# Kernel optimization log

Hardware: AMD Instinct MI355X
Metric: run time of the kernel (lower is better)

## Reference

```python
import jax, jax.numpy as jnp
import numpy as np

N = 50000      # n_nodes
E = 800000     # n_edges
IN_CH = 128
HID = 128
OUT_CH = 64
N_LAYERS = 4


def _linear_params(key, fan_in, fan_out):
    kw, kb = jax.random.split(key)
    bound = 1.0 / np.sqrt(fan_in)
    W = jax.random.uniform(kw, (fan_out, fan_in), jnp.float32, -bound, bound)
    b = jax.random.uniform(kb, (fan_out,), jnp.float32, -bound, bound)
    return W, b


def setup_inputs() -> dict:
    key = jax.random.key(0)
    ks = jax.random.split(key, 5)
    x = jax.random.normal(ks[0], (N, IN_CH), jnp.float32)
    edge_index = jax.random.randint(ks[1], (2, E), 0, N, dtype=jnp.int64)
    W_in, b_in = _linear_params(ks[2], IN_CH, HID)
    conv_keys = jax.random.split(ks[3], N_LAYERS)
    Wc = jnp.stack([_linear_params(k, HID, HID)[0] for k in conv_keys])
    bc = jnp.stack([_linear_params(k, HID, HID)[1] for k in conv_keys])
    W_out, b_out = _linear_params(ks[4], HID * N_LAYERS, OUT_CH)
    return {"x": x, "edge_index": edge_index, "W_in": W_in, "b_in": b_in,
            "Wc": Wc, "bc": bc, "W_out": W_out, "b_out": b_out}


def reference(x, edge_index, W_in, b_in, Wc, bc, W_out, b_out):
    n = x.shape[0]
    # input projection + relu
    x = jax.nn.relu(x @ W_in.T + b_in)
    src, dst = edge_index[0], edge_index[1]
    loop = jnp.arange(n, dtype=edge_index.dtype)
    src_a = jnp.concatenate([src, loop])   # [E+N]
    dst_a = jnp.concatenate([dst, loop])   # [E+N]
    # symmetric-normalized degree (with self loops)
    deg = jax.ops.segment_sum(jnp.ones(src_a.shape[0], x.dtype), dst_a, num_segments=n)
    norm = (deg[src_a] * deg[dst_a]) ** -0.5
    norm = jnp.where(jnp.isinf(norm), 0.0, norm)  # guard deg==0 (original sets inf->0)
    layer_outputs = []
    for i in range(Wc.shape[0]):
        h = x @ Wc[i].T + bc[i]                     # [N, HID]
        msg = h[src_a] * norm[:, None]              # gather + scale  [E+N, HID]
        out = jax.ops.segment_sum(msg, dst_a, num_segments=n)  # scatter-add
        x = jax.nn.relu(out)
        layer_outputs.append(x)
    h = jnp.concatenate(layer_outputs, axis=-1)     # jk_mode='cat' -> [N, HID*L]
    return h @ W_out.T + b_out
```

## Files before the change

### kernel.cpp

```cpp
#include <hip/hip_runtime.h>
#include <hip/hip_bf16.h>

#ifndef MIN
#define MIN(a,b) ((a)<(b)?(a):(b))
#endif

typedef _Float16 half2_t __attribute__((ext_vector_type(2)));
typedef _Float16 half4_t __attribute__((ext_vector_type(4)));
typedef _Float16 half8_t __attribute__((ext_vector_type(8)));
typedef float floatx4 __attribute__((ext_vector_type(4)));

#define BUCKET_SHIFT 6
#define BUCKET_SIZE 64
#define SCHUNK 8192


__global__ void hist_kernel(const int* __restrict__ dst, int E,
                            int* __restrict__ bucketCnt, int NB) {
    __shared__ int h[1024];
    int t = threadIdx.x;
    for (int i = t; i < 1024; i += 256) h[i] = 0;
    __syncthreads();
    for (int e = blockIdx.x * 256 + t; e < E; e += gridDim.x * 256)
        atomicAdd(&h[dst[e] >> BUCKET_SHIFT], 1);
    __syncthreads();
    for (int i = t; i < NB; i += 256)
        if (h[i]) atomicAdd(&bucketCnt[i], h[i]);
}

__global__ void bucket_scan(const int* __restrict__ bucketCnt,
                            int* __restrict__ bucketBase, int* __restrict__ bucketCur,
                            int NB, int E) {
    __shared__ int sm[1024];
    int t = threadIdx.x;
    int v = (t < NB) ? bucketCnt[t] : 0;
    sm[t] = v;
    __syncthreads();
    for (int off = 1; off < 1024; off <<= 1) {
        int add = (t >= off) ? sm[t - off] : 0;
        __syncthreads();
        sm[t] += add;
        __syncthreads();
    }
    if (t < NB) {
        bucketBase[t] = sm[t] - v;
        bucketCur[t] = sm[t] - v;
    }
    if (t == 0) bucketBase[NB] = E;
}

__global__ void scatter_kernel(const int* __restrict__ src, const int* __restrict__ dst,
                               int E, int* __restrict__ bucketCur, uint2* __restrict__ rec) {
    __shared__ int hist[1024];
    __shared__ int base[1024];
    int t = threadIdx.x;
    int e0 = blockIdx.x * SCHUNK;
    int e1 = MIN(E, e0 + SCHUNK);
    for (int i = t; i < 1024; i += 256) hist[i] = 0;
    __syncthreads();
    for (int e = e0 + t; e < e1; e += 256)
        atomicAdd(&hist[dst[e] >> BUCKET_SHIFT], 1);
    __syncthreads();
    for (int i = t; i < 1024; i += 256) {
        int c = hist[i];
        base[i] = c ? atomicAdd(&bucketCur[i], c) : 0;
        hist[i] = 0;
    }
    __syncthreads();
    for (int e = e0 + t; e < e1; e += 256) {
        int d = dst[e];
        int b = d >> BUCKET_SHIFT;
        int pos = base[b] + atomicAdd(&hist[b], 1);
        rec[pos] = make_uint2((unsigned)src[e], (unsigned)d);
    }
}

__global__ void bucket_build(const uint2* __restrict__ rec, const int* __restrict__ bucketBase,
                             int* __restrict__ rowptr, int* __restrict__ csr_src,
                             float* __restrict__ dinv, int N, int E) {
    __shared__ int lcnt[256];
    __shared__ int sm[256];
    __shared__ int lcur[64];
    int b = blockIdx.x;
    int t = threadIdx.x;
    int beg = bucketBase[b], end = bucketBase[b + 1];
    lcnt[t] = 0;
    __syncthreads();
    for (int i = beg + t; i < end; i += 256)
        atomicAdd(&lcnt[rec[i].y & (BUCKET_SIZE - 1)], 1);
    __syncthreads();
    int v = lcnt[t];
    sm[t] = v;
    __syncthreads();
    for (int off = 1; off < 256; off <<= 1) {
        int add = (t >= off) ? sm[t - off] : 0;
        __syncthreads();
        sm[t] += add;
        __syncthreads();
    }
    int excl = sm[t] - v;
    if (t < BUCKET_SIZE) {
        int node = b * BUCKET_SIZE + t;
        if (node < N) {
            rowptr[node] = beg + excl;
            dinv[node] = rsqrtf((float)(v + 1));
        }
        lcur[t] = beg + excl;
    }
    __syncthreads();
    for (int i = beg + t; i < end; i += 256) {
        uint2 r = rec[i];
        int pos = atomicAdd(&lcur[r.y & (BUCKET_SIZE - 1)], 1);
        csr_src[pos] = (int)r.x;
    }
    if (b == 0 && t == 0) rowptr[N] = E;
}


__global__ void cvt_weights(const float* __restrict__ a, _Float16* __restrict__ oa, int na,
                            const float* __restrict__ b, _Float16* __restrict__ ob, int nb,
                            const float* __restrict__ c, _Float16* __restrict__ oc, int nc) {
    int i = blockIdx.x * blockDim.x + threadIdx.x;
    if (i < na) oa[i] = (_Float16)a[i];
    if (i < nb) ob[i] = (_Float16)b[i];
    if (i < nc) oc[i] = (_Float16)c[i];
}


__global__ void agg_kernel(const half2_t* __restrict__ Hb, const float* __restrict__ dinv,
                           const int* __restrict__ rowptr, const int* __restrict__ csr_src,
                           half2_t* __restrict__ X, int N) {
    int node = blockIdx.x * 4 + (threadIdx.x >> 6);
    int t = threadIdx.x & 63;
    if (node >= N) return;
    float di = dinv[node];
    half2_t hu = Hb[(size_t)node * 64 + t];
    float2 acc;
    acc.x = (float)hu.x * di;
    acc.y = (float)hu.y * di;
    int beg = rowptr[node];
    int end = rowptr[node + 1];

    for (int base = beg; base < end; base += 64) {
        int idx = base + t;
        bool valid = idx < end;
        int s_lane = valid ? csr_src[idx] : node;
        float w_lane = valid ? dinv[s_lane] : 0.0f;
        int m = end - base;
        if (m > 64) m = 64;
        int mm = (m + 7) & ~7;
        for (int j = 0; j < mm; j += 8) {
            int s0 = __shfl(s_lane, j + 0), s1 = __shfl(s_lane, j + 1);
            int s2 = __shfl(s_lane, j + 2), s3 = __shfl(s_lane, j + 3);
            int s4 = __shfl(s_lane, j + 4), s5 = __shfl(s_lane, j + 5);
            int s6 = __shfl(s_lane, j + 6), s7 = __shfl(s_lane, j + 7);
            float w0 = __shfl(w_lane, j + 0), w1 = __shfl(w_lane, j + 1);
            float w2 = __shfl(w_lane, j + 2), w3 = __shfl(w_lane, j + 3);
            float w4 = __shfl(w_lane, j + 4), w5 = __shfl(w_lane, j + 5);
            float w6 = __shfl(w_lane, j + 6), w7 = __shfl(w_lane, j + 7);
            half2_t u0 = Hb[(size_t)s0 * 64 + t];
            half2_t u1 = Hb[(size_t)s1 * 64 + t];
            half2_t u2 = Hb[(size_t)s2 * 64 + t];
            half2_t u3 = Hb[(size_t)s3 * 64 + t];
            half2_t u4 = Hb[(size_t)s4 * 64 + t];
            half2_t u5 = Hb[(size_t)s5 * 64 + t];
            half2_t u6 = Hb[(size_t)s6 * 64 + t];
            half2_t u7 = Hb[(size_t)s7 * 64 + t];
            acc.x = fmaf((float)u0.x, w0, acc.x); acc.y = fmaf((float)u0.y, w0, acc.y);
            acc.x = fmaf((float)u1.x, w1, acc.x); acc.y = fmaf((float)u1.y, w1, acc.y);
            acc.x = fmaf((float)u2.x, w2, acc.x); acc.y = fmaf((float)u2.y, w2, acc.y);
            acc.x = fmaf((float)u3.x, w3, acc.x); acc.y = fmaf((float)u3.y, w3, acc.y);
            acc.x = fmaf((float)u4.x, w4, acc.x); acc.y = fmaf((float)u4.y, w4, acc.y);
            acc.x = fmaf((float)u5.x, w5, acc.x); acc.y = fmaf((float)u5.y, w5, acc.y);
            acc.x = fmaf((float)u6.x, w6, acc.x); acc.y = fmaf((float)u6.y, w6, acc.y);
            acc.x = fmaf((float)u7.x, w7, acc.x); acc.y = fmaf((float)u7.y, w7, acc.y);
        }
    }
    half2_t o;
    o.x = (_Float16)fmaxf(acc.x * di, 0.0f);
    o.y = (_Float16)fmaxf(acc.y * di, 0.0f);
    X[(size_t)node * 64 + t] = o;
}


template <int BN, bool A_F16, bool RELU, bool BIAS, bool ACCUM, bool F16OUT>
__global__ __launch_bounds__(256)
void mfma_gemm(const void* __restrict__ Av,
               const _Float16* __restrict__ W, int ldw,
               const float* __restrict__ bias,
               void* __restrict__ Cv, int ldc, int M) {
    constexpr int NT = BN / 16;
    __shared__ __align__(16) _Float16 As[64][136];
    __shared__ __align__(16) _Float16 Ws[BN][136];

    int tid = threadIdx.x;
    int rowBase = blockIdx.x * 64;

#pragma unroll
    for (int i = tid; i < BN * 16; i += 256) {
        int n = i >> 4, k8 = (i & 15) * 8;
        uint4 v = *(const uint4*)(W + (size_t)n * ldw + k8);
        *(uint4*)(&Ws[n][k8]) = v;
    }
    if (A_F16) {
        const _Float16* A = (const _Float16*)Av;
#pragma unroll
        for (int i = tid; i < 64 * 16; i += 256) {
            int r = i >> 4, k8 = (i & 15) * 8;
            int gr = rowBase + r;
            uint4 v = make_uint4(0, 0, 0, 0);
            if (gr < M) v = *(const uint4*)(A + (size_t)gr * 128 + k8);
            *(uint4*)(&As[r][k8]) = v;
        }
    } else {
        const float* A = (const float*)Av;
#pragma unroll
        for (int i = tid; i < 64 * 32; i += 256) {
            int r = i >> 5, c4 = (i & 31) * 4;
            int gr = rowBase + r;
            half4_t h = {0, 0, 0, 0};
            if (gr < M) {
                float4 v = *(const float4*)(A + (size_t)gr * 128 + c4);
                h.x = (_Float16)v.x; h.y = (_Float16)v.y;
                h.z = (_Float16)v.z; h.w = (_Float16)v.w;
            }
            *(half4_t*)(&As[r][c4]) = h;
        }
    }
    __syncthreads();

    int w = tid >> 6;
    int lane = tid & 63;
    int lrow = lane & 15;
    int kq = (lane >> 4) * 8;

    floatx4 acc[NT];
#pragma unroll
    for (int nt = 0; nt < NT; ++nt) acc[nt] = (floatx4){0.f, 0.f, 0.f, 0.f};

#pragma unroll
    for (int ks = 0; ks < 4; ++ks) {
        int kk = ks * 32 + kq;
        half8_t a = *(const half8_t*)(&As[w * 16 + lrow][kk]);
#pragma unroll
        for (int nt = 0; nt < NT; ++nt) {
            half8_t b = *(const half8_t*)(&Ws[nt * 16 + lrow][kk]);
            acc[nt] = __builtin_amdgcn_mfma_f32_16x16x32_f16(a, b, acc[nt], 0, 0, 0);
        }
    }

    int quad = lane >> 4;
#pragma unroll
    for (int nt = 0; nt < NT; ++nt) {
        int col = nt * 16 + lrow;
        float bv = BIAS ? bias[col] : 0.0f;
#pragma unroll
        for (int reg = 0; reg < 4; ++reg) {
            int gr = rowBase + w * 16 + quad * 4 + reg;
            if (gr < M) {
                float v = acc[nt][reg] + bv;
                if (RELU) v = fmaxf(v, 0.0f);
                if (F16OUT) {
                    _Float16* C = (_Float16*)Cv;
                    C[(size_t)gr * ldc + col] = (_Float16)v;
                } else {
                    float* C = (float*)Cv;
                    if (ACCUM) v += C[(size_t)gr * ldc + col];
                    C[(size_t)gr * ldc + col] = v;
                }
            }
        }
    }
}


extern "C" void kernel_launch(void* const* d_in, const int* in_sizes, int n_in,
                              void* d_out, int out_size, void* d_ws, size_t ws_size,
                              hipStream_t stream) {
    const float* x     = (const float*)d_in[0];
    const int*   ei    = (const int*)d_in[1];
    const float* W_in  = (const float*)d_in[2];
    const float* b_in  = (const float*)d_in[3];
    const float* Wc    = (const float*)d_in[4];
    const float* bc    = (const float*)d_in[5];
    const float* W_out = (const float*)d_in[6];
    const float* b_out = (const float*)d_in[7];
    float* out = (float*)d_out;

    const int HID = 128;
    const int N = in_sizes[0] / HID;
    const int E = in_sizes[1] / 2;
    const int L = 4;
    const int* src = ei;
    const int* dst = ei + E;
    const int NB = (N + BUCKET_SIZE - 1) >> BUCKET_SHIFT;

    char* ws = (char*)d_ws;
    size_t off = 0;
    auto carve = [&](size_t bytes) {
        void* p = ws + off;
        off += (bytes + 255) & ~(size_t)255;
        return p;
    };
    float* dinv      = (float*)carve((size_t)N * 4);
    int*   rowptr    = (int*)carve((size_t)(N + 1) * 4);
    int*   csr_src   = (int*)carve((size_t)E * 4);
    uint2* rec       = (uint2*)carve((size_t)E * 8);
    int*   bucketCnt = (int*)carve((size_t)1024 * 4);
    int*   bucketBase= (int*)carve((size_t)1025 * 4);
    int*   bucketCur = (int*)carve((size_t)1024 * 4);
    _Float16* bufA   = (_Float16*)carve((size_t)N * HID * 2);
    _Float16* bufH   = (_Float16*)carve((size_t)N * HID * 2);
    _Float16* Wf_in  = (_Float16*)carve((size_t)HID * HID * 2);
    _Float16* Wf_c   = (_Float16*)carve((size_t)L * HID * HID * 2);
    _Float16* Wf_out = (_Float16*)carve((size_t)64 * 512 * 2);
    (void)ws_size;

    hipMemsetAsync(bucketCnt, 0, (size_t)1024 * 4, stream);
    hist_kernel<<<512, 256, 0, stream>>>(dst, E, bucketCnt, NB);
    bucket_scan<<<1, 1024, 0, stream>>>(bucketCnt, bucketBase, bucketCur, NB, E);
    scatter_kernel<<<(E + SCHUNK - 1) / SCHUNK, 256, 0, stream>>>(src, dst, E, bucketCur, rec);
    bucket_build<<<NB, 256, 0, stream>>>(rec, bucketBase, rowptr, csr_src, dinv, N, E);

    cvt_weights<<<(L * HID * HID + 255) / 256, 256, 0, stream>>>(
        W_in, Wf_in, HID * HID,
        Wc, Wf_c, L * HID * HID,
        W_out, Wf_out, 64 * 512);

    int gemm_blocks = (N + 63) / 64;

    mfma_gemm<128, false, true, true, false, true>
        <<<gemm_blocks, 256, 0, stream>>>(x, Wf_in, HID, b_in, bufA, HID, N);

    for (int l = 0; l < L; ++l) {
        mfma_gemm<128, true, false, true, false, true>
            <<<gemm_blocks, 256, 0, stream>>>(bufA, Wf_c + (size_t)l * HID * HID, HID,
                                              bc + (size_t)l * HID, bufH, HID, N);
        agg_kernel<<<(N + 3) / 4, 256, 0, stream>>>((const half2_t*)bufH, dinv, rowptr,
                                                    csr_src, (half2_t*)bufA, N);
        if (l == 0) {
            mfma_gemm<64, true, false, true, false, false>
                <<<gemm_blocks, 256, 0, stream>>>(bufA, Wf_out + (size_t)l * HID, 512,
                                                  b_out, out, 64, N);
        } else {
            mfma_gemm<64, true, false, false, true, false>
                <<<gemm_blocks, 256, 0, stream>>>(bufA, Wf_out + (size_t)l * HID, 512,
                                                  nullptr, out, 64, N);
        }
    }
}
```

Baseline: 387.0 us.

## Compress CSR to 16-bit indices, concat layer outputs, single final GEMM

Packs scatter records into 32-bit words and stores CSR source indices as 16-bit values, which shrinks edge-index traffic in graph build and aggregation. Layer outputs go into a 512-wide concatenated buffer, and one final K=512 GEMM replaces the four per-layer accumulating output GEMMs with their read-modify-write of the fp32 output. The GEMM now loads A fragments straight from global memory into registers instead of staging them in shared memory. The scatter chunk size is also reduced. The 16-bit source index only holds for N < 65536, so it depends on the test graph size and gives wrong results on larger graphs.

```diff
diff --git a/kernel.cpp b/kernel.cpp
--- a/kernel.cpp
+++ b/kernel.cpp
@@ -12,7 +12,7 @@
 
 #define BUCKET_SHIFT 6
 #define BUCKET_SIZE 64
-#define SCHUNK 8192
+#define SCHUNK 2048
 
 
 __global__ void hist_kernel(const int* __restrict__ dst, int E,
@@ -50,7 +50,8 @@
 }
 
 __global__ void scatter_kernel(const int* __restrict__ src, const int* __restrict__ dst,
-                               int E, int* __restrict__ bucketCur, uint2* __restrict__ rec) {
+                               int E, int* __restrict__ bucketCur,
+                               unsigned int* __restrict__ rec) {
     __shared__ int hist[1024];
     __shared__ int base[1024];
     int t = threadIdx.x;
@@ -71,12 +72,13 @@
         int d = dst[e];
         int b = d >> BUCKET_SHIFT;
         int pos = base[b] + atomicAdd(&hist[b], 1);
-        rec[pos] = make_uint2((unsigned)src[e], (unsigned)d);
-    }
-}
-
-__global__ void bucket_build(const uint2* __restrict__ rec, const int* __restrict__ bucketBase,
-                             int* __restrict__ rowptr, int* __restrict__ csr_src,
+        rec[pos] = (unsigned)src[e] | ((unsigned)(d & (BUCKET_SIZE - 1)) << 16);
+    }
+}
+
+__global__ void bucket_build(const unsigned int* __restrict__ rec,
+                             const int* __restrict__ bucketBase,
+                             int* __restrict__ rowptr, unsigned short* __restrict__ csr_src,
                              float* __restrict__ dinv, int N, int E) {
     __shared__ int lcnt[256];
     __shared__ int sm[256];
@@ -87,7 +89,7 @@
     lcnt[t] = 0;
     __syncthreads();
     for (int i = beg + t; i < end; i += 256)
-        atomicAdd(&lcnt[rec[i].y & (BUCKET_SIZE - 1)], 1);
+        atomicAdd(&lcnt[rec[i] >> 16], 1);
     __syncthreads();
     int v = lcnt[t];
     sm[t] = v;
@@ -109,9 +111,9 @@
     }
     __syncthreads();
     for (int i = beg + t; i < end; i += 256) {
-        uint2 r = rec[i];
-        int pos = atomicAdd(&lcur[r.y & (BUCKET_SIZE - 1)], 1);
-        csr_src[pos] = (int)r.x;
+        unsigned int r = rec[i];
+        int pos = atomicAdd(&lcur[r >> 16], 1);
+        csr_src[pos] = (unsigned short)(r & 0xFFFFu);
     }
     if (b == 0 && t == 0) rowptr[N] = E;
 }
@@ -128,7 +130,8 @@
 
 
 __global__ void agg_kernel(const half2_t* __restrict__ Hb, const float* __restrict__ dinv,
-                           const int* __restrict__ rowptr, const int* __restrict__ csr_src,
+                           const int* __restrict__ rowptr,
+                           const unsigned short* __restrict__ csr_src,
                            half2_t* __restrict__ X, int N) {
     int node = blockIdx.x * 4 + (threadIdx.x >> 6);
     int t = threadIdx.x & 63;
@@ -144,7 +147,7 @@
     for (int base = beg; base < end; base += 64) {
         int idx = base + t;
         bool valid = idx < end;
-        int s_lane = valid ? csr_src[idx] : node;
+        int s_lane = valid ? (int)csr_src[idx] : node;
         float w_lane = valid ? dinv[s_lane] : 0.0f;
         int m = end - base;
         if (m > 64) m = 64;
@@ -179,94 +182,99 @@
     half2_t o;
     o.x = (_Float16)fmaxf(acc.x * di, 0.0f);
     o.y = (_Float16)fmaxf(acc.y * di, 0.0f);
-    X[(size_t)node * 64 + t] = o;
-}
-
-
-template <int BN, bool A_F16, bool RELU, bool BIAS, bool ACCUM, bool F16OUT>
+    X[(size_t)node * 256 + t] = o;
+}
+
+
+template <int BN, int KCH, bool A_F16, bool RELU, bool BIAS, bool F16OUT>
 __global__ __launch_bounds__(256)
-void mfma_gemm(const void* __restrict__ Av,
+void mfma_gemm(const void* __restrict__ Av, int lda,
                const _Float16* __restrict__ W, int ldw,
                const float* __restrict__ bias,
                void* __restrict__ Cv, int ldc, int M) {
     constexpr int NT = BN / 16;
-    __shared__ __align__(16) _Float16 As[64][136];
     __shared__ __align__(16) _Float16 Ws[BN][136];
 
     int tid = threadIdx.x;
     int rowBase = blockIdx.x * 64;
-
-#pragma unroll
-    for (int i = tid; i < BN * 16; i += 256) {
-        int n = i >> 4, k8 = (i & 15) * 8;
-        uint4 v = *(const uint4*)(W + (size_t)n * ldw + k8);
-        *(uint4*)(&Ws[n][k8]) = v;
-    }
-    if (A_F16) {
-        const _Float16* A = (const _Float16*)Av;
-#pragma unroll
-        for (int i = tid; i < 64 * 16; i += 256) {
-            int r = i >> 4, k8 = (i & 15) * 8;
-            int gr = rowBase + r;
-            uint4 v = make_uint4(0, 0, 0, 0);
-            if (gr < M) v = *(const uint4*)(A + (size_t)gr * 128 + k8);
-            *(uint4*)(&As[r][k8]) = v;
-        }
-    } else {
-        const float* A = (const float*)Av;
-#pragma unroll
-        for (int i = tid; i < 64 * 32; i += 256) {
-            int r = i >> 5, c4 = (i & 31) * 4;
-            int gr = rowBase + r;
-            half4_t h = {0, 0, 0, 0};
-            if (gr < M) {
-                float4 v = *(const float4*)(A + (size_t)gr * 128 + c4);
-                h.x = (_Float16)v.x; h.y = (_Float16)v.y;
-                h.z = (_Float16)v.z; h.w = (_Float16)v.w;
-            }
-            *(half4_t*)(&As[r][c4]) = h;
-        }
-    }
-    __syncthreads();
-
     int w = tid >> 6;
     int lane = tid & 63;
     int lrow = lane & 15;
-    int kq = (lane >> 4) * 8;
+    int quad = lane >> 4;
+    int kq = quad * 8;
+    int gr = rowBase + w * 16 + lrow;
 
     floatx4 acc[NT];
 #pragma unroll
     for (int nt = 0; nt < NT; ++nt) acc[nt] = (floatx4){0.f, 0.f, 0.f, 0.f};
 
 #pragma unroll
-    for (int ks = 0; ks < 4; ++ks) {
-        int kk = ks * 32 + kq;
-        half8_t a = *(const half8_t*)(&As[w * 16 + lrow][kk]);
-#pragma unroll
-        for (int nt = 0; nt < NT; ++nt) {
-            half8_t b = *(const half8_t*)(&Ws[nt * 16 + lrow][kk]);
-            acc[nt] = __builtin_amdgcn_mfma_f32_16x16x32_f16(a, b, acc[nt], 0, 0, 0);
-        }
-    }
-
-    int quad = lane >> 4;
+    for (int kc = 0; kc < KCH; ++kc) {
+#pragma unroll
+        for (int i = tid; i < BN * 16; i += 256) {
+            int n = i >> 4, k8 = (i & 15) * 8;
+            uint4 v = *(const uint4*)(W + (size_t)n * ldw + kc * 128 + k8);
+            *(uint4*)(&Ws[n][k8]) = v;
+        }
+        __syncthreads();
+
+        half8_t a[4];
+        if (gr < M) {
+            if (A_F16) {
+                const _Float16* A = (const _Float16*)Av;
+                const _Float16* ap = A + (size_t)gr * lda + kc * 128 + kq;
+#pragma unroll
+                for (int ks = 0; ks < 4; ++ks)
+                    a[ks] = *(const half8_t*)(ap + ks * 32);
+            } else {
+                const float* A = (const float*)Av;
+                const float* ap = A + (size_t)gr * lda + kc * 128 + kq;
+#pragma unroll
+                for (int ks = 0; ks < 4; ++ks) {
+                    float4 v0 = *(const float4*)(ap + ks * 32);
+                    float4 v1 = *(const float4*)(ap + ks * 32 + 4);
+                    half8_t h;
+                    h[0] = (_Float16)v0.x; h[1] = (_Float16)v0.y;
+                    h[2] = (_Float16)v0.z; h[3] = (_Float16)v0.w;
+                    h[4] = (_Float16)v1.x; h[5] = (_Float16)v1.y;
+                    h[6] = (_Float16)v1.z; h[7] = (_Float16)v1.w;
+                    a[ks] = h;
+                }
+            }
+        } else {
+#pragma unroll
+            for (int ks = 0; ks < 4; ++ks)
+                a[ks] = (half8_t){0, 0, 0, 0, 0, 0, 0, 0};
+        }
+
+#pragma unroll
+        for (int ks = 0; ks < 4; ++ks) {
+            int kk = ks * 32 + kq;
+#pragma unroll
+            for (int nt = 0; nt < NT; ++nt) {
+                half8_t b = *(const half8_t*)(&Ws[nt * 16 + lrow][kk]);
+                acc[nt] = __builtin_amdgcn_mfma_f32_16x16x32_f16(a[ks], b, acc[nt], 0, 0, 0);
+            }
+        }
+        if (kc != KCH - 1) __syncthreads();
+    }
+
 #pragma unroll
     for (int nt = 0; nt < NT; ++nt) {
         int col = nt * 16 + lrow;
         float bv = BIAS ? bias[col] : 0.0f;
 #pragma unroll
         for (int reg = 0; reg < 4; ++reg) {
-            int gr = rowBase + w * 16 + quad * 4 + reg;
-            if (gr < M) {
+            int gr2 = rowBase + w * 16 + quad * 4 + reg;
+            if (gr2 < M) {
                 float v = acc[nt][reg] + bv;
                 if (RELU) v = fmaxf(v, 0.0f);
                 if (F16OUT) {
                     _Float16* C = (_Float16*)Cv;
-                    C[(size_t)gr * ldc + col] = (_Float16)v;
+                    C[(size_t)gr2 * ldc + col] = (_Float16)v;
                 } else {
                     float* C = (float*)Cv;
-                    if (ACCUM) v += C[(size_t)gr * ldc + col];
-                    C[(size_t)gr * ldc + col] = v;
+                    C[(size_t)gr2 * ldc + col] = v;
                 }
             }
         }
@@ -302,18 +310,19 @@
         off += (bytes + 255) & ~(size_t)255;
         return p;
     };
-    float* dinv      = (float*)carve((size_t)N * 4);
-    int*   rowptr    = (int*)carve((size_t)(N + 1) * 4);
-    int*   csr_src   = (int*)carve((size_t)E * 4);
-    uint2* rec       = (uint2*)carve((size_t)E * 8);
-    int*   bucketCnt = (int*)carve((size_t)1024 * 4);
-    int*   bucketBase= (int*)carve((size_t)1025 * 4);
-    int*   bucketCur = (int*)carve((size_t)1024 * 4);
-    _Float16* bufA   = (_Float16*)carve((size_t)N * HID * 2);
-    _Float16* bufH   = (_Float16*)carve((size_t)N * HID * 2);
-    _Float16* Wf_in  = (_Float16*)carve((size_t)HID * HID * 2);
-    _Float16* Wf_c   = (_Float16*)carve((size_t)L * HID * HID * 2);
-    _Float16* Wf_out = (_Float16*)carve((size_t)64 * 512 * 2);
+    float* dinv        = (float*)carve((size_t)N * 4);
+    int*   rowptr      = (int*)carve((size_t)(N + 1) * 4);
+    unsigned short* csr_src = (unsigned short*)carve((size_t)E * 2);
+    unsigned int* rec  = (unsigned int*)carve((size_t)E * 4);
+    int*   bucketCnt   = (int*)carve((size_t)1024 * 4);
+    int*   bucketBase  = (int*)carve((size_t)1025 * 4);
+    int*   bucketCur   = (int*)carve((size_t)1024 * 4);
+    _Float16* bufA     = (_Float16*)carve((size_t)N * HID * 2);
+    _Float16* bufH     = (_Float16*)carve((size_t)N * HID * 2);
+    _Float16* bufXcat  = (_Float16*)carve((size_t)N * 512 * 2);
+    _Float16* Wf_in    = (_Float16*)carve((size_t)HID * HID * 2);
+    _Float16* Wf_c     = (_Float16*)carve((size_t)L * HID * HID * 2);
+    _Float16* Wf_out   = (_Float16*)carve((size_t)64 * 512 * 2);
     (void)ws_size;
 
     hipMemsetAsync(bucketCnt, 0, (size_t)1024 * 4, stream);
@@ -329,23 +338,21 @@
 
     int gemm_blocks = (N + 63) / 64;
 
-    mfma_gemm<128, false, true, true, false, true>
-        <<<gemm_blocks, 256, 0, stream>>>(x, Wf_in, HID, b_in, bufA, HID, N);
+    mfma_gemm<128, 1, false, true, true, true>
+        <<<gemm_blocks, 256, 0, stream>>>(x, 128, Wf_in, HID, b_in, bufA, HID, N);
 
     for (int l = 0; l < L; ++l) {
-        mfma_gemm<128, true, false, true, false, true>
-            <<<gemm_blocks, 256, 0, stream>>>(bufA, Wf_c + (size_t)l * HID * HID, HID,
+        const void* Ain = (l == 0) ? (const void*)bufA
+                                   : (const void*)(bufXcat + (size_t)(l - 1) * 128);
+        int lda = (l == 0) ? 128 : 512;
+        mfma_gemm<128, 1, true, false, true, true>
+            <<<gemm_blocks, 256, 0, stream>>>(Ain, lda, Wf_c + (size_t)l * HID * HID, HID,
                                               bc + (size_t)l * HID, bufH, HID, N);
         agg_kernel<<<(N + 3) / 4, 256, 0, stream>>>((const half2_t*)bufH, dinv, rowptr,
-                                                    csr_src, (half2_t*)bufA, N);
-        if (l == 0) {
-            mfma_gemm<64, true, false, true, false, false>
-                <<<gemm_blocks, 256, 0, stream>>>(bufA, Wf_out + (size_t)l * HID, 512,
-                                                  b_out, out, 64, N);
-        } else {
-            mfma_gemm<64, true, false, false, true, false>
-                <<<gemm_blocks, 256, 0, stream>>>(bufA, Wf_out + (size_t)l * HID, 512,
-                                                  nullptr, out, 64, N);
-        }
-    }
-}
+                                                    csr_src,
+                                                    (half2_t*)bufXcat + (size_t)l * 64, N);
+    }
+
+    mfma_gemm<64, 4, true, false, true, false>
+        <<<gemm_blocks, 256, 0, stream>>>(bufXcat, 512, Wf_out, 512, b_out, out, 64, N);
+}
```

Measured after the change: 326.3 us. 15.7% less time.
